# Performance work log

Measured on AMD Instinct MI355X. Metric: run time of the kernel, lower is better.

The kernel has to match this reference:

```python
import jax, jax.numpy as jnp
import numpy as np

EPS = 1e-08
LAM = 0.01


def setup_inputs() -> dict:
    key = jax.random.key(0)
    k1, k2, k3 = jax.random.split(key, 3)
    BS, L, N = 256, 2048, 128
    pred_weights = jax.random.normal(k1, (BS, L, N), dtype=jnp.float32)
    # positive prices in [0.5, 1.5) to avoid div-by-zero / inf
    price_list = jax.random.uniform(k2, (BS, L + 1, N), dtype=jnp.float32, minval=0.5, maxval=1.5)
    # valid lengths in [2, L] (torch.var is unbiased -> need n >= 2)
    pred_sz = jax.random.randint(k3, (BS, 1), 2, L + 1, dtype=jnp.int64)
    return {"pred_weights": pred_weights, "price_list": price_list, "pred_sz": pred_sz}


def reference(pred_weights, price_list, pred_sz):
    P_i = price_list[:, :-1, :]  # [BS, L, N] past prices
    P_j = price_list[:, 1:, :]   # [BS, L, N] future prices
    r = jnp.nan_to_num((P_j - P_i) / P_i)
    r = r * (r <= 2)             # zero out returns > 2 (outlier mask)

    L = r.shape[1]
    Rp = jnp.sum(pred_weights[:, :L, :] * r, axis=-1)  # [BS, L] portfolio returns

    n = pred_sz.reshape(-1).astype(Rp.dtype)                       # [BS]
    mask = (jnp.arange(L)[None, :] < pred_sz.reshape(-1, 1)).astype(Rp.dtype)  # [BS, L]

    expected_Rp = jnp.sum(Rp * mask, axis=1) / n                   # masked mean
    centered = (Rp - expected_Rp[:, None]) * mask
    variance_Rp = jnp.sum(centered * centered, axis=1) / (n - 1)   # unbiased var (torch.var default)

    denom = jnp.sqrt(variance_Rp + EPS)
    sharpe = expected_Rp / denom
    sharpe_list = expected_Rp - LAM / denom

    return (-jnp.mean(sharpe_list), -jnp.mean(sharpe), jnp.mean(expected_Rp), jnp.mean(variance_Rp))
```

## Files before the change

### kernel.cpp

```cpp
#include <hip/hip_runtime.h>

#define EPS 1e-8f
#define LAM 0.01f

constexpr int BS = 256;
constexpr int L  = 2048;
constexpr int N  = 128;
constexpr int CHUNK  = 256;
constexpr int NCHUNK = L / CHUNK;


__global__ __launch_bounds__(256) void rp_kernel(
    const float* __restrict__ w,
    const float* __restrict__ price,
    const int*  __restrict__ pred_sz,
    float* __restrict__ ws)
{
    const int b     = blockIdx.x / NCHUNK;
    const int chunk = blockIdx.x % NCHUNK;
    const int n     = pred_sz[b];

    const int start = chunk * CHUNK;
    if (start >= n) return;
    const int end = min(start + CHUNK, n);

    const int tid  = threadIdx.x;
    const int grp  = tid >> 5;
    const int lane = tid & 31;

    float s1 = 0.0f, s2 = 0.0f;

    #pragma unroll
    for (int batch = 0; batch < 2; ++batch) {
        const int rs = start + grp * 32 + batch * 16;

        float A[16];
        #pragma unroll
        for (int r = 0; r < 16; ++r) A[r] = 0.0f;

        if (rs < end) {
            const float* wp = w     + ((size_t)b * L       + rs) * N + lane * 4;
            const float* pp = price + ((size_t)b * (L + 1) + rs) * N + lane * 4;

            float4 pv = *reinterpret_cast<const float4*>(pp);
            #pragma unroll
            for (int r = 0; r < 16; ++r) {
                if (rs + r < end) {
                    const float4 pj = *reinterpret_cast<const float4*>(pp + (size_t)(r + 1) * N);
                    const float4 wv = *reinterpret_cast<const float4*>(wp + (size_t)r * N);

                    float r0 = (pj.x - pv.x) * __builtin_amdgcn_rcpf(pv.x);
                    float r1 = (pj.y - pv.y) * __builtin_amdgcn_rcpf(pv.y);
                    float r2 = (pj.z - pv.z) * __builtin_amdgcn_rcpf(pv.z);
                    float r3 = (pj.w - pv.w) * __builtin_amdgcn_rcpf(pv.w);
                    r0 = (r0 <= 2.0f) ? r0 : 0.0f;
                    r1 = (r1 <= 2.0f) ? r1 : 0.0f;
                    r2 = (r2 <= 2.0f) ? r2 : 0.0f;
                    r3 = (r3 <= 2.0f) ? r3 : 0.0f;

                    A[r] = wv.x * r0 + wv.y * r1 + wv.z * r2 + wv.w * r3;
                    pv = pj;
                }
            }
        }

        #pragma unroll
        for (int k = 0; k < 4; ++k) {
            const int  m  = 1 << k;
            const bool hi = (lane & m) != 0;
            #pragma unroll
            for (int t = 0; t < (8 >> k); ++t) {
                const float send = hi ? A[2 * t] : A[2 * t + 1];
                const float recv = __shfl_xor(send, m);
                A[t] = (hi ? A[2 * t + 1] : A[2 * t]) + recv;
            }
        }
        const float v = A[0] + __shfl_xor(A[0], 16);
        const float vm = (lane & 16) ? 0.0f : v;
        s1 += vm;
        s2 += vm * vm;
    }

    #pragma unroll
    for (int m = 1; m < 32; m <<= 1) {
        s1 += __shfl_xor(s1, m);
        s2 += __shfl_xor(s2, m);
    }
    __shared__ float ls1[8], ls2[8];
    if (lane == 0) { ls1[grp] = s1; ls2[grp] = s2; }
    __syncthreads();
    if (tid == 0) {
        float t1 = 0.0f, t2 = 0.0f;
        #pragma unroll
        for (int i = 0; i < 8; ++i) { t1 += ls1[i]; t2 += ls2[i]; }
        ws[b * NCHUNK + chunk]               = t1;
        ws[BS * NCHUNK + b * NCHUNK + chunk] = t2;
    }
}

__global__ __launch_bounds__(256) void final_kernel(
    const float* __restrict__ ws,
    const int*  __restrict__ pred_sz,
    float* __restrict__ out)
{
    const int b = threadIdx.x;
    const int ni = pred_sz[b];
    const int nc = (ni + CHUNK - 1) / CHUNK;

    float s1 = 0.0f, s2 = 0.0f;
    for (int c = 0; c < nc; ++c) {
        s1 += ws[b * NCHUNK + c];
        s2 += ws[BS * NCHUNK + b * NCHUNK + c];
    }

    const float n     = (float)ni;
    const float E     = s1 / n;
    const float var   = (s2 - n * E * E) / (n - 1.0f);
    const float denom = sqrtf(var + EPS);
    const float sharpe      = E / denom;
    const float sharpe_list = E - LAM / denom;

    __shared__ float red[4][BS];
    red[0][b] = sharpe_list;
    red[1][b] = sharpe;
    red[2][b] = E;
    red[3][b] = var;
    __syncthreads();

    #pragma unroll
    for (int s = BS / 2; s > 0; s >>= 1) {
        if (b < s) {
            red[0][b] += red[0][b + s];
            red[1][b] += red[1][b + s];
            red[2][b] += red[2][b + s];
            red[3][b] += red[3][b + s];
        }
        __syncthreads();
    }

    if (b == 0) {
        out[0] = -red[0][0] / (float)BS;
        out[1] = -red[1][0] / (float)BS;
        out[2] =  red[2][0] / (float)BS;
        out[3] =  red[3][0] / (float)BS;
    }
}

extern "C" void kernel_launch(void* const* d_in, const int* in_sizes, int n_in,
                              void* d_out, int out_size, void* d_ws, size_t ws_size,
                              hipStream_t stream) {
    const float* w     = (const float*)d_in[0];
    const float* price = (const float*)d_in[1];
    const int*   psz   = (const int*)d_in[2];
    float* out = (float*)d_out;
    float* ws  = (float*)d_ws;

    rp_kernel<<<BS * NCHUNK, 256, 0, stream>>>(w, price, psz, ws);
    final_kernel<<<1, BS, 0, stream>>>(ws, psz, out);
}
```

Before: 75.21 us.

## Halve row chunk size and split full-tile fast path from masked tail

Reduces CHUNK from 256 to 128 rows so each 32-lane group processes 16 rows instead of 32, doubling the block count for more parallelism and finer skipping of rows past pred_sz. Full 16-row tiles take a branch-free path that processes rows in two halves of 8 with a shorter transpose-reduce, which lowers register pressure. Partial tiles use a simple per-row loop with a full warp reduction. In exchange there are more blocks, more partial-sum writes and more final-kernel reads, and the tail path is slower per row.

```diff
diff --git a/kernel.cpp b/kernel.cpp
--- a/kernel.cpp
+++ b/kernel.cpp
@@ -6,9 +6,25 @@
 constexpr int BS = 256;
 constexpr int L  = 2048;
 constexpr int N  = 128;
-constexpr int CHUNK  = 256;
+constexpr int CHUNK  = 128;
 constexpr int NCHUNK = L / CHUNK;
 
+
+__device__ __forceinline__ float4 ld4(const float* p) {
+    return *reinterpret_cast<const float4*>(p);
+}
+
+__device__ __forceinline__ float rowdot(const float4 wv, const float4 pi, const float4 pj) {
+    float r0 = (pj.x - pi.x) * __builtin_amdgcn_rcpf(pi.x);
+    float r1 = (pj.y - pi.y) * __builtin_amdgcn_rcpf(pi.y);
+    float r2 = (pj.z - pi.z) * __builtin_amdgcn_rcpf(pi.z);
+    float r3 = (pj.w - pi.w) * __builtin_amdgcn_rcpf(pi.w);
+    r0 = (r0 <= 2.0f) ? r0 : 0.0f;
+    r1 = (r1 <= 2.0f) ? r1 : 0.0f;
+    r2 = (r2 <= 2.0f) ? r2 : 0.0f;
+    r3 = (r3 <= 2.0f) ? r3 : 0.0f;
+    return wv.x * r0 + wv.y * r1 + wv.z * r2 + wv.w * r3;
+}
 
 __global__ __launch_bounds__(256) void rp_kernel(
     const float* __restrict__ w,
@@ -28,57 +44,58 @@
     const int grp  = tid >> 5;
     const int lane = tid & 31;
 
+    const int rs = start + grp * 16;
+    const int re = min(rs + 16, end);
+
     float s1 = 0.0f, s2 = 0.0f;
 
-    #pragma unroll
-    for (int batch = 0; batch < 2; ++batch) {
-        const int rs = start + grp * 32 + batch * 16;
+    if (re - rs == 16) {
+        const float* wp = w     + ((size_t)b * L       + rs) * N + lane * 4;
+        const float* pp = price + ((size_t)b * (L + 1) + rs) * N + lane * 4;
 
-        float A[16];
+        float4 pv = ld4(pp);
         #pragma unroll
-        for (int r = 0; r < 16; ++r) A[r] = 0.0f;
+        for (int half = 0; half < 2; ++half) {
+            float A[8];
+            #pragma unroll
+            for (int r = 0; r < 8; ++r) {
+                const int rr = half * 8 + r;
+                const float4 pj = ld4(pp + (size_t)(rr + 1) * N);
+                const float4 wv = ld4(wp + (size_t)rr * N);
+                A[r] = rowdot(wv, pv, pj);
+                pv = pj;
+            }
 
-        if (rs < end) {
-            const float* wp = w     + ((size_t)b * L       + rs) * N + lane * 4;
-            const float* pp = price + ((size_t)b * (L + 1) + rs) * N + lane * 4;
-
-            float4 pv = *reinterpret_cast<const float4*>(pp);
             #pragma unroll
-            for (int r = 0; r < 16; ++r) {
-                if (rs + r < end) {
-                    const float4 pj = *reinterpret_cast<const float4*>(pp + (size_t)(r + 1) * N);
-                    const float4 wv = *reinterpret_cast<const float4*>(wp + (size_t)r * N);
-
-                    float r0 = (pj.x - pv.x) * __builtin_amdgcn_rcpf(pv.x);
-                    float r1 = (pj.y - pv.y) * __builtin_amdgcn_rcpf(pv.y);
-                    float r2 = (pj.z - pv.z) * __builtin_amdgcn_rcpf(pv.z);
-                    float r3 = (pj.w - pv.w) * __builtin_amdgcn_rcpf(pv.w);
-                    r0 = (r0 <= 2.0f) ? r0 : 0.0f;
-                    r1 = (r1 <= 2.0f) ? r1 : 0.0f;
-                    r2 = (r2 <= 2.0f) ? r2 : 0.0f;
-                    r3 = (r3 <= 2.0f) ? r3 : 0.0f;
-
-                    A[r] = wv.x * r0 + wv.y * r1 + wv.z * r2 + wv.w * r3;
-                    pv = pj;
+            for (int k = 0; k < 3; ++k) {
+                const int  m  = 1 << k;
+                const bool hi = (lane & m) != 0;
+                #pragma unroll
+                for (int t = 0; t < (4 >> k); ++t) {
+                    const float send = hi ? A[2 * t] : A[2 * t + 1];
+                    const float recv = __shfl_xor(send, m);
+                    A[t] = (hi ? A[2 * t + 1] : A[2 * t]) + recv;
                 }
             }
+            float v = A[0] + __shfl_xor(A[0], 8);
+            v += __shfl_xor(v, 16);
+            const float vm = ((lane & 24) == 0) ? v : 0.0f;
+            s1 += vm;
+            s2 += vm * vm;
         }
-
-        #pragma unroll
-        for (int k = 0; k < 4; ++k) {
-            const int  m  = 1 << k;
-            const bool hi = (lane & m) != 0;
+    } else if (rs < end) {
+        const float* wp = w     + ((size_t)b * L       + rs) * N + lane * 4;
+        const float* pp = price + ((size_t)b * (L + 1) + rs) * N + lane * 4;
+        for (int l = rs; l < re; ++l, wp += N, pp += N) {
+            const float4 pi = ld4(pp);
+            const float4 pj = ld4(pp + N);
+            const float4 wv = ld4(wp);
+            float acc = rowdot(wv, pi, pj);
             #pragma unroll
-            for (int t = 0; t < (8 >> k); ++t) {
-                const float send = hi ? A[2 * t] : A[2 * t + 1];
-                const float recv = __shfl_xor(send, m);
-                A[t] = (hi ? A[2 * t + 1] : A[2 * t]) + recv;
-            }
+            for (int m = 1; m < 32; m <<= 1)
+                acc += __shfl_xor(acc, m);
+            if (lane == 0) { s1 += acc; s2 += acc * acc; }
         }
-        const float v = A[0] + __shfl_xor(A[0], 16);
-        const float vm = (lane & 16) ? 0.0f : v;
-        s1 += vm;
-        s2 += vm * vm;
     }
 
     #pragma unroll
```

Result: faster. 68.43 us (-9.0%).
